# Kernel tuning notes

Measured on AMD Instinct MI355X. Metric: run time of the kernel, lower is better.

## Reference

```python
import jax, jax.numpy as jnp
import numpy as np

B, D, H = 8192, 1024, 1024


def setup_inputs() -> dict:
    key = jax.random.key(0)
    k1, k2, k3, k4, k5 = jax.random.split(key, 5)
    # binary spins/pixels as float (teacher-forced input)
    x = (jax.random.uniform(k1, (B, D)) < 0.5).astype(jnp.float32)
    # params mimicking kaiming-uniform scale
    V = jax.random.normal(k2, (D, H), dtype=jnp.float32) * np.float32(1.0 / np.sqrt(H))
    b = jax.random.normal(k3, (D,), dtype=jnp.float32) * np.float32(1.0 / np.sqrt(H))
    W = jax.random.normal(k4, (H, D), dtype=jnp.float32) * np.float32(1.0 / np.sqrt(D))
    c = jax.random.normal(k5, (H,), dtype=jnp.float32) * np.float32(1.0 / np.sqrt(D))
    return {"x": x, "V": V, "b": b, "W": W, "c": c}


def reference(x, V, b, W, c):
    # NADE forward (teacher forcing): sequential over D output dims.
    # carry a: (H, B) pre-activation of hidden state
    a0 = jnp.broadcast_to(c[:, None], (H, x.shape[0]))

    def step(a, inp):
        v_d, w_d, b_d, x_d = inp  # (H,), (H,), (), (B,)
        h = jax.nn.sigmoid(a)                              # (H, B)
        p = jax.nn.sigmoid(b_d + jnp.einsum('hb,h->b', h, v_d))  # (B,)
        a = a + w_d[:, None] * x_d[None, :]                # rank-1 state update
        return a, p

    # per-step inputs, leading dim D
    _, ps = jax.lax.scan(step, a0, (V, W.T, b, x.T))       # ps: (D, B)
    return ps.T                                            # x_hat: (B, D)
```

## Files before the change

### kernel.cpp

```cpp
#include <hip/hip_runtime.h>
#include <stdint.h>

#define Bq 8192
#define Dq 1024
#define Hq 1024
#define GROUP 2
#define NGROUP (Dq / GROUP)

typedef __fp16 half2_t __attribute__((ext_vector_type(2)));

static constexpr float NLOG2E = -1.4426950408889634f;

__device__ __forceinline__ void gl_lds16(const void* g, void* l) {
  __builtin_amdgcn_global_load_lds(
      (const __attribute__((address_space(1))) uint32_t*)g,
      (__attribute__((address_space(3))) uint32_t*)l, 16, 0, 0);
}

template <int CTRL>
__device__ __forceinline__ float dppadd(float v) {
  const int x = __builtin_bit_cast(int, v);
  const int y = __builtin_amdgcn_update_dpp(x, x, CTRL, 0xF, 0xF, false);
  return v + __builtin_bit_cast(float, y);
}

template <int OFF>
__device__ __forceinline__ float swzadd(float v) {
  const int y = __builtin_amdgcn_ds_swizzle(__builtin_bit_cast(int, v), OFF);
  return v + __builtin_bit_cast(float, y);
}

__global__ __launch_bounds__(256) void prepEF(const float* __restrict__ W,
                                              __fp16* __restrict__ EF) {
  __shared__ float tile[32][33];
  const int tx = threadIdx.x, ty = threadIdx.y;
  const int bx = blockIdx.x, by = blockIdx.y;
#pragma unroll
  for (int i = 0; i < 4; ++i)
    tile[ty + i * 8][tx] = W[(size_t)(by * 32 + ty + i * 8) * Dq + bx * 32 + tx];
  __syncthreads();
#pragma unroll
  for (int i = 0; i < 4; ++i) {
    const int d = bx * 32 + ty + i * 8;
    const int h = by * 32 + tx;
    const float E = exp2f(tile[tx][ty + i * 8] * NLOG2E);
    EF[(size_t)d * 2048 + h] = (__fp16)E;
    EF[(size_t)d * 2048 + 1024 + h] = (__fp16)(1.0f - E);
  }
}

__global__ __launch_bounds__(256) void convV(const float* __restrict__ V,
                                             uint32_t* __restrict__ Vh) {
  const int i = blockIdx.x * 256 + threadIdx.x;
  const float4 v = reinterpret_cast<const float4*>(V)[i];
  half2_t h0 = __builtin_amdgcn_cvt_pkrtz(v.x * NLOG2E, v.y * NLOG2E);
  half2_t h1 = __builtin_amdgcn_cvt_pkrtz(v.z * NLOG2E, v.w * NLOG2E);
  uint2 pk;
  pk.x = __builtin_bit_cast(uint32_t, h0);
  pk.y = __builtin_bit_cast(uint32_t, h1);
  reinterpret_cast<uint2*>(Vh)[i] = pk;
}

__global__ __launch_bounds__(256, 4) void nade_fwd(
    const float* __restrict__ x, const uint32_t* __restrict__ Vh,
    const float* __restrict__ bvec, const uint32_t* __restrict__ EF,
    const float* __restrict__ cvec, float* __restrict__ out) {
  __shared__ __align__(16) uint32_t Vs[2][GROUP][Hq / 2];
  __shared__ __align__(16) uint32_t Es[2][GROUP][Hq];

  const int tid = threadIdx.x;
  const int wave = tid >> 6;
  const int lane = tid & 63;
  const bool odd = lane & 1;
  const int b0 = blockIdx.x * 8 + wave * 2;

  half2_t yy[2][8], hh[2][8];
  {
    float cv[16];
#pragma unroll
    for (int q = 0; q < 2; ++q) {
      *reinterpret_cast<float4*>(&cv[8 * q]) =
          *reinterpret_cast<const float4*>(&cvec[512 * q + 8 * lane]);
      *reinterpret_cast<float4*>(&cv[8 * q + 4]) =
          *reinterpret_cast<const float4*>(&cvec[512 * q + 8 * lane + 4]);
    }
#pragma unroll
    for (int j = 0; j < 8; ++j) {
      const float y0 = 1.0f + __builtin_amdgcn_exp2f(cv[2 * j] * NLOG2E);
      const float y1 = 1.0f + __builtin_amdgcn_exp2f(cv[2 * j + 1] * NLOG2E);
      const half2_t yp = __builtin_amdgcn_cvt_pkrtz(y0, y1);
      const half2_t hp = __builtin_amdgcn_cvt_pkrtz(
          __builtin_amdgcn_rcpf(y0), __builtin_amdgcn_rcpf(y1));
#pragma unroll
      for (int k = 0; k < 2; ++k) {
        yy[k][j] = yp;
        hh[k][j] = hp;
      }
    }
  }

  auto stage = [&](int d0, int buf) {
    const char* vsrc = (const char*)Vh + (size_t)d0 * 2048;
    gl_lds16(vsrc + wave * 1024 + lane * 16, (char*)&Vs[buf][0][0] + wave * 1024);
    const char* esrc = (const char*)EF + (size_t)d0 * 4096;
#pragma unroll
    for (int q = 0; q < 2; ++q)
      gl_lds16(esrc + q * 4096 + wave * 1024 + lane * 16,
               (char*)&Es[buf][0][0] + q * 4096 + wave * 1024);
  };

  stage(0, 0);

  unsigned long long xm[2];
  float breg = 0.f;
  float po0, po1, po2, po3;
  const half2_t two2 = {(__fp16)2.0f, (__fp16)2.0f};

  __syncthreads();

#define UPD(k)                                                               \
  {                                                                          \
    _Pragma("unroll") for (int j = 0; j < 8; ++j) {                          \
      yy[k][j] = yy[k][j] * e[j] + f[j];                   \
      const half2_t t = two2 - hh[k][j] * yy[k][j];        \
      hh[k][j] = hh[k][j] * t;                             \
    }                                                                        \
  }

#define STEP(CUR, SS, D, PO)                                                 \
  {                                                                          \
    const int dl = (D)&63;                                                   \
    const char* vp = (const char*)&Vs[CUR][SS][0];                           \
    const uint4 v0 = *reinterpret_cast<const uint4*>(vp + 16 * lane);        \
    const uint4 v1 = *reinterpret_cast<const uint4*>(vp + 1024 + 16 * lane); \
    half2_t vh[8];                                                           \
    vh[0] = __builtin_bit_cast(half2_t, v0.x);                               \
    vh[1] = __builtin_bit_cast(half2_t, v0.y);                               \
    vh[2] = __builtin_bit_cast(half2_t, v0.z);                               \
    vh[3] = __builtin_bit_cast(half2_t, v0.w);                               \
    vh[4] = __builtin_bit_cast(half2_t, v1.x);                               \
    vh[5] = __builtin_bit_cast(half2_t, v1.y);                               \
    vh[6] = __builtin_bit_cast(half2_t, v1.z);                               \
    vh[7] = __builtin_bit_cast(half2_t, v1.w);                               \
    float dot0 = 0.f, dot1 = 0.f;                                            \
    _Pragma("unroll") for (int p = 0; p < 8; ++p) {                          \
      dot0 = __builtin_amdgcn_fdot2(hh[0][p], vh[p], dot0, false);           \
      dot1 = __builtin_amdgcn_fdot2(hh[1][p], vh[p], dot1, false);           \
    }                                                                        \
    dot0 = dppadd<0xB1>(dot0);                                               \
    dot1 = dppadd<0xB1>(dot1);                                               \
    float s = odd ? dot1 : dot0;                                             \
    s = dppadd<0x4E>(s);                                                     \
    s = swzadd<0x101F>(s);                                                   \
    s = swzadd<0x201F>(s);                                                   \
    s = swzadd<0x401F>(s);                                                   \
    s += __shfl_xor(s, 32);                                                  \
    const float bd = __shfl(breg, dl);                                       \
    PO = __builtin_amdgcn_rcpf(1.0f + __builtin_amdgcn_exp2f(bd + s));       \
    const bool a0 = (xm[0] >> dl) & 1;                                       \
    const bool a1 = (xm[1] >> dl) & 1;                                       \
    if (a0 | a1) {                                                           \
      const char* ep = (const char*)&Es[CUR][SS][0];                         \
      const uint4 e0 = *reinterpret_cast<const uint4*>(ep + 16 * lane);      \
      const uint4 e1 = *reinterpret_cast<const uint4*>(ep + 1024 + 16 * lane); \
      const uint4 f0 = *reinterpret_cast<const uint4*>(ep + 2048 + 16 * lane); \
      const uint4 f1 = *reinterpret_cast<const uint4*>(ep + 3072 + 16 * lane); \
      half2_t e[8], f[8];                                                    \
      e[0] = __builtin_bit_cast(half2_t, e0.x);                              \
      e[1] = __builtin_bit_cast(half2_t, e0.y);                              \
      e[2] = __builtin_bit_cast(half2_t, e0.z);                              \
      e[3] = __builtin_bit_cast(half2_t, e0.w);                              \
      e[4] = __builtin_bit_cast(half2_t, e1.x);                              \
      e[5] = __builtin_bit_cast(half2_t, e1.y);                              \
      e[6] = __builtin_bit_cast(half2_t, e1.z);                              \
      e[7] = __builtin_bit_cast(half2_t, e1.w);                              \
      f[0] = __builtin_bit_cast(half2_t, f0.x);                              \
      f[1] = __builtin_bit_cast(half2_t, f0.y);                              \
      f[2] = __builtin_bit_cast(half2_t, f0.z);                              \
      f[3] = __builtin_bit_cast(half2_t, f0.w);                              \
      f[4] = __builtin_bit_cast(half2_t, f1.x);                              \
      f[5] = __builtin_bit_cast(half2_t, f1.y);                              \
      f[6] = __builtin_bit_cast(half2_t, f1.z);                              \
      f[7] = __builtin_bit_cast(half2_t, f1.w);                              \
      if (a0) UPD(0)                                                         \
      if (a1) UPD(1)                                                         \
    }                                                                        \
  }

  for (int gg = 0; gg < NGROUP; gg += 2) {
    if ((gg & 31) == 0) {
#pragma unroll
      for (int k = 0; k < 2; ++k) {
        const float xv = x[(size_t)(b0 + k) * Dq + 2 * gg + lane];
        xm[k] = __ballot(xv != 0.0f);
      }
      breg = bvec[2 * gg + lane] * NLOG2E;
    }

    stage(2 * (gg + 1), 1);
    STEP(0, 0, 2 * gg, po0)
    STEP(0, 1, 2 * gg + 1, po1)
    __syncthreads();

    if (gg + 2 < NGROUP) stage(2 * (gg + 2), 0);
    STEP(1, 0, 2 * gg + 2, po2)
    STEP(1, 1, 2 * gg + 3, po3)
    __syncthreads();

    if (lane < 2) {
      *reinterpret_cast<float4*>(&out[(size_t)(b0 + lane) * Dq + 2 * gg]) =
          make_float4(po0, po1, po2, po3);
    }
  }
#undef STEP
#undef UPD
}

extern "C" void kernel_launch(void* const* d_in, const int* in_sizes, int n_in,
                              void* d_out, int out_size, void* d_ws, size_t ws_size,
                              hipStream_t stream) {
  (void)in_sizes; (void)n_in; (void)out_size; (void)ws_size;
  const float* x = (const float*)d_in[0];
  const float* V = (const float*)d_in[1];
  const float* b = (const float*)d_in[2];
  const float* W = (const float*)d_in[3];
  const float* c = (const float*)d_in[4];
  float* out = (float*)d_out;
  __fp16* EF = (__fp16*)d_ws;
  uint32_t* Vh = (uint32_t*)((char*)d_ws + (size_t)Dq * 4096);

  prepEF<<<dim3(Dq / 32, Hq / 32), dim3(32, 8), 0, stream>>>(W, EF);
  convV<<<(Dq * Hq / 4) / 256, 256, 0, stream>>>(V, Vh);
  nade_fwd<<<Bq / 8, 256, 0, stream>>>(x, Vh, b, (const uint32_t*)EF, c, out);
}
```

Measured before the change: 833.3 us.

## Process one batch row per wave and drop the F table from staging

Each wave now tracks one batch row instead of two, so the grid doubles to B/4 blocks and launch bounds rise to allow eight blocks per CU. The precomputed 1-E table is removed and the state update is rewritten as (y-1)*E+1, which halves the per-step E traffic to LDS and the LDS footprint. The bias broadcast uses readlane instead of a shuffle. The trade-off is that each staged V/E tile is now reused by half as many rows per block, so total global-to-LDS traffic rises, and the extra subtraction in fp16 may change rounding.

```diff
diff --git a/kernel.cpp b/kernel.cpp
--- a/kernel.cpp
+++ b/kernel.cpp
@@ -30,8 +30,8 @@
   return v + __builtin_bit_cast(float, y);
 }
 
-__global__ __launch_bounds__(256) void prepEF(const float* __restrict__ W,
-                                              __fp16* __restrict__ EF) {
+__global__ __launch_bounds__(256) void prepE(const float* __restrict__ W,
+                                             __fp16* __restrict__ Eh) {
   __shared__ float tile[32][33];
   const int tx = threadIdx.x, ty = threadIdx.y;
   const int bx = blockIdx.x, by = blockIdx.y;
@@ -43,9 +43,7 @@
   for (int i = 0; i < 4; ++i) {
     const int d = bx * 32 + ty + i * 8;
     const int h = by * 32 + tx;
-    const float E = exp2f(tile[tx][ty + i * 8] * NLOG2E);
-    EF[(size_t)d * 2048 + h] = (__fp16)E;
-    EF[(size_t)d * 2048 + 1024 + h] = (__fp16)(1.0f - E);
+    Eh[(size_t)d * Hq + h] = (__fp16)exp2f(tile[tx][ty + i * 8] * NLOG2E);
   }
 }
 
@@ -61,76 +59,57 @@
   reinterpret_cast<uint2*>(Vh)[i] = pk;
 }
 
-__global__ __launch_bounds__(256, 4) void nade_fwd(
+__global__ __launch_bounds__(256, 8) void nade_fwd(
     const float* __restrict__ x, const uint32_t* __restrict__ Vh,
-    const float* __restrict__ bvec, const uint32_t* __restrict__ EF,
+    const float* __restrict__ bvec, const uint32_t* __restrict__ Eh,
     const float* __restrict__ cvec, float* __restrict__ out) {
   __shared__ __align__(16) uint32_t Vs[2][GROUP][Hq / 2];
-  __shared__ __align__(16) uint32_t Es[2][GROUP][Hq];
+  __shared__ __align__(16) uint32_t Es[2][GROUP][Hq / 2];
 
   const int tid = threadIdx.x;
   const int wave = tid >> 6;
   const int lane = tid & 63;
-  const bool odd = lane & 1;
-  const int b0 = blockIdx.x * 8 + wave * 2;
-
-  half2_t yy[2][8], hh[2][8];
-  {
-    float cv[16];
-#pragma unroll
-    for (int q = 0; q < 2; ++q) {
-      *reinterpret_cast<float4*>(&cv[8 * q]) =
-          *reinterpret_cast<const float4*>(&cvec[512 * q + 8 * lane]);
-      *reinterpret_cast<float4*>(&cv[8 * q + 4]) =
-          *reinterpret_cast<const float4*>(&cvec[512 * q + 8 * lane + 4]);
-    }
-#pragma unroll
-    for (int j = 0; j < 8; ++j) {
+  const int b0 = blockIdx.x * 4 + wave;
+
+  half2_t yy[8], hh[8];
+#pragma unroll
+  for (int q = 0; q < 2; ++q) {
+    float cv[8];
+    *reinterpret_cast<float4*>(&cv[0]) =
+        *reinterpret_cast<const float4*>(&cvec[512 * q + 8 * lane]);
+    *reinterpret_cast<float4*>(&cv[4]) =
+        *reinterpret_cast<const float4*>(&cvec[512 * q + 8 * lane + 4]);
+#pragma unroll
+    for (int j = 0; j < 4; ++j) {
       const float y0 = 1.0f + __builtin_amdgcn_exp2f(cv[2 * j] * NLOG2E);
       const float y1 = 1.0f + __builtin_amdgcn_exp2f(cv[2 * j + 1] * NLOG2E);
-      const half2_t yp = __builtin_amdgcn_cvt_pkrtz(y0, y1);
-      const half2_t hp = __builtin_amdgcn_cvt_pkrtz(
+      yy[4 * q + j] = __builtin_amdgcn_cvt_pkrtz(y0, y1);
+      hh[4 * q + j] = __builtin_amdgcn_cvt_pkrtz(
           __builtin_amdgcn_rcpf(y0), __builtin_amdgcn_rcpf(y1));
-#pragma unroll
-      for (int k = 0; k < 2; ++k) {
-        yy[k][j] = yp;
-        hh[k][j] = hp;
-      }
     }
   }
 
   auto stage = [&](int d0, int buf) {
-    const char* vsrc = (const char*)Vh + (size_t)d0 * 2048;
-    gl_lds16(vsrc + wave * 1024 + lane * 16, (char*)&Vs[buf][0][0] + wave * 1024);
-    const char* esrc = (const char*)EF + (size_t)d0 * 4096;
-#pragma unroll
-    for (int q = 0; q < 2; ++q)
-      gl_lds16(esrc + q * 4096 + wave * 1024 + lane * 16,
-               (char*)&Es[buf][0][0] + q * 4096 + wave * 1024);
+    gl_lds16((const char*)Vh + (size_t)d0 * 2048 + tid * 16,
+             (char*)&Vs[buf][0][0] + wave * 1024);
+    gl_lds16((const char*)Eh + (size_t)d0 * 2048 + tid * 16,
+             (char*)&Es[buf][0][0] + wave * 1024);
   };
 
   stage(0, 0);
 
-  unsigned long long xm[2];
+  unsigned long long xm = 0;
   float breg = 0.f;
   float po0, po1, po2, po3;
+  const half2_t one2 = {(__fp16)1.0f, (__fp16)1.0f};
   const half2_t two2 = {(__fp16)2.0f, (__fp16)2.0f};
 
   __syncthreads();
-
-#define UPD(k)                                                               \
-  {                                                                          \
-    _Pragma("unroll") for (int j = 0; j < 8; ++j) {                          \
-      yy[k][j] = yy[k][j] * e[j] + f[j];                   \
-      const half2_t t = two2 - hh[k][j] * yy[k][j];        \
-      hh[k][j] = hh[k][j] * t;                             \
-    }                                                                        \
-  }
 
 #define STEP(CUR, SS, D, PO)                                                 \
   {                                                                          \
     const int dl = (D)&63;                                                   \
-    const char* vp = (const char*)&Vs[CUR][SS][0];                           \
+    const char* vp = (const char*)&Vs[0][0][0] + (CUR * GROUP + SS) * 2048;  \
     const uint4 v0 = *reinterpret_cast<const uint4*>(vp + 16 * lane);        \
     const uint4 v1 = *reinterpret_cast<const uint4*>(vp + 1024 + 16 * lane); \
     half2_t vh[8];                                                           \
@@ -142,30 +121,24 @@
     vh[5] = __builtin_bit_cast(half2_t, v1.y);                               \
     vh[6] = __builtin_bit_cast(half2_t, v1.z);                               \
     vh[7] = __builtin_bit_cast(half2_t, v1.w);                               \
-    float dot0 = 0.f, dot1 = 0.f;                                            \
+    float s = 0.f;                                                           \
     _Pragma("unroll") for (int p = 0; p < 8; ++p) {                          \
-      dot0 = __builtin_amdgcn_fdot2(hh[0][p], vh[p], dot0, false);           \
-      dot1 = __builtin_amdgcn_fdot2(hh[1][p], vh[p], dot1, false);           \
+      s = __builtin_amdgcn_fdot2(hh[p], vh[p], s, false);                    \
     }                                                                        \
-    dot0 = dppadd<0xB1>(dot0);                                               \
-    dot1 = dppadd<0xB1>(dot1);                                               \
-    float s = odd ? dot1 : dot0;                                             \
-    s = dppadd<0x4E>(s);                                                     \
-    s = swzadd<0x101F>(s);                                                   \
-    s = swzadd<0x201F>(s);                                                   \
-    s = swzadd<0x401F>(s);                                                   \
+    s = dppadd<0xB1>(s);                                           \
+    s = dppadd<0x4E>(s);                                           \
+    s = swzadd<0x101F>(s);                                         \
+    s = swzadd<0x201F>(s);                                         \
+    s = swzadd<0x401F>(s);                                        \
     s += __shfl_xor(s, 32);                                                  \
-    const float bd = __shfl(breg, dl);                                       \
+    const float bd = __builtin_bit_cast(                                     \
+        float, __builtin_amdgcn_readlane(__builtin_bit_cast(int, breg), dl)); \
     PO = __builtin_amdgcn_rcpf(1.0f + __builtin_amdgcn_exp2f(bd + s));       \
-    const bool a0 = (xm[0] >> dl) & 1;                                       \
-    const bool a1 = (xm[1] >> dl) & 1;                                       \
-    if (a0 | a1) {                                                           \
-      const char* ep = (const char*)&Es[CUR][SS][0];                         \
+    if ((xm >> dl) & 1) {                                                    \
+      const char* ep = (const char*)&Es[0][0][0] + (CUR * GROUP + SS) * 2048; \
       const uint4 e0 = *reinterpret_cast<const uint4*>(ep + 16 * lane);      \
       const uint4 e1 = *reinterpret_cast<const uint4*>(ep + 1024 + 16 * lane); \
-      const uint4 f0 = *reinterpret_cast<const uint4*>(ep + 2048 + 16 * lane); \
-      const uint4 f1 = *reinterpret_cast<const uint4*>(ep + 3072 + 16 * lane); \
-      half2_t e[8], f[8];                                                    \
+      half2_t e[8];                                                          \
       e[0] = __builtin_bit_cast(half2_t, e0.x);                              \
       e[1] = __builtin_bit_cast(half2_t, e0.y);                              \
       e[2] = __builtin_bit_cast(half2_t, e0.z);                              \
@@ -174,26 +147,19 @@
       e[5] = __builtin_bit_cast(half2_t, e1.y);                              \
       e[6] = __builtin_bit_cast(half2_t, e1.z);                              \
       e[7] = __builtin_bit_cast(half2_t, e1.w);                              \
-      f[0] = __builtin_bit_cast(half2_t, f0.x);                              \
-      f[1] = __builtin_bit_cast(half2_t, f0.y);                              \
-      f[2] = __builtin_bit_cast(half2_t, f0.z);                              \
-      f[3] = __builtin_bit_cast(half2_t, f0.w);                              \
-      f[4] = __builtin_bit_cast(half2_t, f1.x);                              \
-      f[5] = __builtin_bit_cast(half2_t, f1.y);                              \
-      f[6] = __builtin_bit_cast(half2_t, f1.z);                              \
-      f[7] = __builtin_bit_cast(half2_t, f1.w);                              \
-      if (a0) UPD(0)                                                         \
-      if (a1) UPD(1)                                                         \
+      _Pragma("unroll") for (int j = 0; j < 8; ++j) {                        \
+        const half2_t t = yy[j] - one2;                                      \
+        yy[j] = t * e[j] + one2;                        \
+        const half2_t nt = two2 - hh[j] * yy[j];                             \
+        hh[j] = hh[j] * nt;                        \
+      }                                                                      \
     }                                                                        \
   }
 
   for (int gg = 0; gg < NGROUP; gg += 2) {
     if ((gg & 31) == 0) {
-#pragma unroll
-      for (int k = 0; k < 2; ++k) {
-        const float xv = x[(size_t)(b0 + k) * Dq + 2 * gg + lane];
-        xm[k] = __ballot(xv != 0.0f);
-      }
+      const float xv = x[(size_t)b0 * Dq + 2 * gg + lane];
+      xm = __ballot(xv != 0.0f);
       breg = bvec[2 * gg + lane] * NLOG2E;
     }
 
@@ -207,13 +173,12 @@
     STEP(1, 1, 2 * gg + 3, po3)
     __syncthreads();
 
-    if (lane < 2) {
-      *reinterpret_cast<float4*>(&out[(size_t)(b0 + lane) * Dq + 2 * gg]) =
+    if (lane == 0) {
+      *reinterpret_cast<float4*>(&out[(size_t)b0 * Dq + 2 * gg]) =
           make_float4(po0, po1, po2, po3);
     }
   }
 #undef STEP
-#undef UPD
 }
 
 extern "C" void kernel_launch(void* const* d_in, const int* in_sizes, int n_in,
@@ -226,10 +191,10 @@
   const float* W = (const float*)d_in[3];
   const float* c = (const float*)d_in[4];
   float* out = (float*)d_out;
-  __fp16* EF = (__fp16*)d_ws;
-  uint32_t* Vh = (uint32_t*)((char*)d_ws + (size_t)Dq * 4096);
-
-  prepEF<<<dim3(Dq / 32, Hq / 32), dim3(32, 8), 0, stream>>>(W, EF);
+  __fp16* Eh = (__fp16*)d_ws;
+  uint32_t* Vh = (uint32_t*)((char*)d_ws + (size_t)Dq * Hq * 2);
+
+  prepE<<<dim3(Dq / 32, Hq / 32), dim3(32, 8), 0, stream>>>(W, Eh);
   convV<<<(Dq * Hq / 4) / 256, 256, 0, stream>>>(V, Vh);
-  nade_fwd<<<Bq / 8, 256, 0, stream>>>(x, Vh, b, (const uint32_t*)EF, c, out);
-}
+  nade_fwd<<<Bq / 4, 256, 0, stream>>>(x, Vh, b, (const uint32_t*)Eh, c, out);
+}
```

Measured after the change: 942.1 us. 1.13x slower.
